# Kernel tuning notes

Hardware: AMD Instinct MI355X
Metric: run time of the kernel (lower is better)

## Reference

```python
import jax, jax.numpy as jnp
import numpy as np

B, T, K, H, NH = 16, 2048, 128, 1024, 8
NEG = -jnp.inf


def _ln(x, g, b, eps=1e-5):
    m = x.mean(-1, keepdims=True)
    v = ((x - m) ** 2).mean(-1, keepdims=True)
    return (x - m) * jax.lax.rsqrt(v + eps) * g + b


def _mha(q, k, v, in_w, in_b, out_w, out_b, nh, bias):
    # torch nn.MultiheadAttention (batch_first, eval mode). bias: additive mask (B or 1, 1, Lq, Lk)
    Bq, Lq, Hd = q.shape
    Lk = k.shape[1]
    d = Hd // nh
    wq, wk, wv = in_w[:Hd], in_w[Hd:2 * Hd], in_w[2 * Hd:]
    bq, bk, bv = in_b[:Hd], in_b[Hd:2 * Hd], in_b[2 * Hd:]
    qh = (q @ wq.T + bq).reshape(Bq, Lq, nh, d).transpose(0, 2, 1, 3)
    kh = (k @ wk.T + bk).reshape(Bq, Lk, nh, d).transpose(0, 2, 1, 3)
    vh = (v @ wv.T + bv).reshape(Bq, Lk, nh, d).transpose(0, 2, 1, 3)
    scores = jnp.einsum('bhqd,bhkd->bhqk', qh, kh) * (1.0 / np.sqrt(d)) + bias
    attn = jax.nn.softmax(scores, axis=-1)
    o = jnp.einsum('bhqk,bhkd->bhqd', attn, vh).transpose(0, 2, 1, 3).reshape(Bq, Lq, Hd)
    return o @ out_w.T + out_b


def setup_inputs() -> dict:
    key = jax.random.key(0)
    ks = jax.random.split(key, 12)
    projected = jax.random.normal(ks[0], (B, T, H), dtype=jnp.float32)
    starts = jnp.sort(jax.random.randint(ks[1], (B, K), 0, T - 1), axis=-1)
    widths = jax.random.randint(ks[2], (B, K), 1, 33)
    ends = jnp.minimum(starts + widths, T)
    boundaries = jnp.stack([starts, ends], axis=-1).astype(jnp.int64)
    slot_mask = jnp.ones((B, K), dtype=jnp.float32)
    s = 0.02
    p = {
        'qp_w': jax.random.normal(ks[3], (H, H)) * s, 'qp_b': jnp.zeros((H,)),
        'ca_in_w': jax.random.normal(ks[4], (3 * H, H)) * s, 'ca_in_b': jnp.zeros((3 * H,)),
        'ca_out_w': jax.random.normal(ks[5], (H, H)) * s, 'ca_out_b': jnp.zeros((H,)),
        'cn_g': jnp.ones((H,)), 'cn_b': jnp.zeros((H,)),
        'sa_in_w': jax.random.normal(ks[6], (3 * H, H)) * s, 'sa_in_b': jnp.zeros((3 * H,)),
        'sa_out_w': jax.random.normal(ks[7], (H, H)) * s, 'sa_out_b': jnp.zeros((H,)),
        'on_g': jnp.ones((H,)), 'on_b': jnp.zeros((H,)),
    }
    return {'projected': projected, 'boundaries': boundaries, 'slot_mask': slot_mask, **p}


def reference(projected, boundaries, slot_mask, qp_w, qp_b, ca_in_w, ca_in_b, ca_out_w, ca_out_b,
              cn_g, cn_b, sa_in_w, sa_in_b, sa_out_w, sa_out_b, on_g, on_b):
    Bb, Tt, Hh = projected.shape
    Kk = slot_mask.shape[1]
    tidx = jnp.arange(Tt)
    starts = boundaries[:, :, 0]  # (B,K)
    ends = boundaries[:, :, 1]
    # in-boundary membership: (B,K,T)
    in_bkt = (tidx[None, None, :] >= starts[:, :, None]) & (tidx[None, None, :] < ends[:, :, None])
    valid = slot_mask > 0.5  # (B,K)
    # --- mean-pool init queries ---
    in_slot = (in_bkt & (slot_mask[:, :, None] > 0)).astype(projected.dtype)  # (B,K,T)
    w = in_slot / jnp.clip(in_slot.sum(axis=-1, keepdims=True), 1.0, None)
    init_slots = jnp.einsum('bkt,bth->bkh', w, projected)
    queries = init_slots @ qp_w.T + qp_b
    # --- boundary-masked cross attention (True = blocked) ---
    blocked = ~(in_bkt & valid[:, :, None])  # (B,K,T)
    cross_bias = jnp.where(blocked, NEG, 0.0)[:, None, :, :]  # (B,1,K,T)
    attn_out = _mha(queries, projected, projected, ca_in_w, ca_in_b, ca_out_w, ca_out_b, NH, cross_bias)
    slots = _ln(attn_out + queries, cn_g, cn_b)
    # --- causal self-attention over slots with key padding ---
    causal = jnp.where(jnp.triu(jnp.ones((Kk, Kk), bool), 1), NEG, 0.0)[None, None, :, :]
    pad = jnp.where(slot_mask[:, None, None, :] < 0.5, NEG, 0.0)  # (B,1,1,K)
    ctx = _mha(slots, slots, slots, sa_in_w, sa_in_b, sa_out_w, sa_out_b, NH, causal + pad)
    return _ln(ctx + slots, on_g, on_b)
```

## Files before the change

kernel.cpp:

```cpp
#include <hip/hip_runtime.h>
#include <hip/hip_bf16.h>


#define Bc 16
#define Tc 2048
#define Kc 128
#define Hc 1024
#define NHc 8

typedef unsigned short u16;
typedef __attribute__((ext_vector_type(8))) short short8v;
typedef __attribute__((ext_vector_type(4))) float f32x4;

__device__ __forceinline__ float bf2f(u16 u){ return __uint_as_float(((unsigned)u)<<16); }
__device__ __forceinline__ u16 f2bf(float f){
  unsigned x = __float_as_uint(f);
  return (u16)((x + 0x7fffu + ((x>>16)&1u)) >> 16);
}
__device__ __forceinline__ float4 ld4(const float* p){ return *(const float4*)p; }
__device__ __forceinline__ float ldx(const void* x, size_t idx, bool isbf){
  return isbf ? bf2f(((const u16*)x)[idx]) : ((const float*)x)[idx];
}
__device__ __forceinline__ bool probe_bf(const u16* probe){ return probe[0] == 0x3F80; }

__device__ __forceinline__ void gload_lds16(const u16* g, u16* l){
  __builtin_amdgcn_global_load_lds(
      (const __attribute__((address_space(1))) unsigned int*)g,
      (__attribute__((address_space(3))) unsigned int*)l, 16, 0, 0);
}

struct CvtArgs { const void* src[15]; int n[15]; long long off[15]; int tobf[15]; };

__global__ __launch_bounds__(256) void convert_params(CvtArgs a, float* fbase,
                                                      u16* bbase, const u16* probe)
{
  bool isbf = probe_bf(probe);
  int g = blockIdx.x*256 + threadIdx.x;
  int stride = gridDim.x*256;
  #pragma unroll 1
  for (int seg=0; seg<15; seg++){
    int n = a.n[seg];
    const void* s = a.src[seg];
    if (a.tobf[seg]){
      u16* d = bbase + a.off[seg];
      if (isbf){ const u16* su=(const u16*)s; for (int i=g;i<n;i+=stride) d[i]=su[i]; }
      else     { const float* sf=(const float*)s; for (int i=g;i<n;i+=stride) d[i]=f2bf(sf[i]); }
    } else {
      float* d = fbase + a.off[seg];
      for (int i=g;i<n;i+=stride) d[i] = ldx(s, i, isbf);
    }
  }
}

__global__ __launch_bounds__(256) void transpose_bf(
    const u16* __restrict__ src, u16* __restrict__ dst, int n)
{
  __shared__ u16 t[32][33];
  int bx = blockIdx.x*32, by = blockIdx.y*32;
  int tx = threadIdx.x & 31, ty = threadIdx.x >> 5;
  #pragma unroll
  for (int i=0;i<32;i+=8)
    t[ty+i][tx] = src[(size_t)(by+ty+i)*n + bx+tx];
  __syncthreads();
  #pragma unroll
  for (int i=0;i<32;i+=8)
    dst[(size_t)(bx+ty+i)*n + by+tx] = t[tx][ty+i];
}

__global__ __launch_bounds__(256) void gemm_mfma(
    const u16* __restrict__ A, const u16* __restrict__ W,
    const float* __restrict__ bias, float* __restrict__ Cf, u16* __restrict__ Cb,
    int M, int N, int Kd, int lda, int ldw, int ldc, float alpha,
    int ZH, long long sAb, long long sAh, long long sWb, long long sWh,
    long long sCb, long long sCh, long long sBh)
{
  __shared__ __align__(16) u16 As[128*32];
  __shared__ __align__(16) u16 Bs[128*32];
  int z = blockIdx.z, bi = z / ZH, hi = z % ZH;
  A += (size_t)bi*sAb + (size_t)hi*sAh;
  W += (size_t)bi*sWb + (size_t)hi*sWh;
  int tid = threadIdx.x;
  int m0 = blockIdx.y*128, n0 = blockIdx.x*128;
  int wave = tid >> 6, lane = tid & 63;
  int wm = (wave >> 1)*64, wn = (wave & 1)*64;
  int r = lane & 15, half = lane >> 4;
  int srow = wave*32 + (lane >> 2);
  int skc  = (lane & 3) << 3;
  u16* ldsA = &As[wave*1024];
  u16* ldsB = &Bs[wave*1024];

  f32x4 acc[4][4] = {};

  for (int k0 = 0; k0 < Kd; k0 += 32){
    gload_lds16(A + (size_t)(m0+srow   )*lda + k0 + skc, ldsA);
    gload_lds16(A + (size_t)(m0+srow+16)*lda + k0 + skc, ldsA + 512);
    gload_lds16(W + (size_t)(n0+srow   )*ldw + k0 + skc, ldsB);
    gload_lds16(W + (size_t)(n0+srow+16)*ldw + k0 + skc, ldsB + 512);
    __syncthreads();
    short8v a[4], b[4];
    #pragma unroll
    for (int mi=0;mi<4;mi++)
      a[mi] = *(const short8v*)&As[(wm+mi*16+r)*32 + half*8];
    #pragma unroll
    for (int ni=0;ni<4;ni++)
      b[ni] = *(const short8v*)&Bs[(wn+ni*16+r)*32 + half*8];
    #pragma unroll
    for (int mi=0;mi<4;mi++)
      #pragma unroll
      for (int ni=0;ni<4;ni++)
        acc[mi][ni] = __builtin_amdgcn_mfma_f32_16x16x32_bf16(a[mi], b[ni], acc[mi][ni], 0, 0, 0);
    __syncthreads();
  }

  float* Cfp = Cf ? Cf + (size_t)bi*sCb + (size_t)hi*sCh : nullptr;
  u16*   Cbp = Cb ? Cb + (size_t)bi*sCb + (size_t)hi*sCh : nullptr;
  #pragma unroll
  for (int ni=0;ni<4;ni++){
    int col = n0 + wn + ni*16 + r;
    float bvv = bias ? bias[(size_t)hi*sBh + col] : 0.f;
    #pragma unroll
    for (int mi=0;mi<4;mi++){
      #pragma unroll
      for (int d=0;d<4;d++){
        int rowc = m0 + wm + mi*16 + half*4 + d;
        float o = alpha*acc[mi][ni][d] + bvv;
        if (Cfp) Cfp[(size_t)rowc*ldc + col] = o;
        if (Cbp) Cbp[(size_t)rowc*ldc + col] = f2bf(o);
      }
    }
  }
}

__global__ __launch_bounds__(256) void gemm_nt(
    const float* __restrict__ A, const float* __restrict__ W,
    const float* __restrict__ bias, float* __restrict__ C,
    int M, int N, int Kd, int lda, int ldw, int ldc, float alpha,
    int ZH, long long sAb, long long sAh, long long sWb, long long sWh,
    long long sCb, long long sCh, long long sBh)
{
  __shared__ float As[16][68];
  __shared__ float Bs[16][68];
  int z = blockIdx.z, bi = z / ZH, hi = z % ZH;
  A += (size_t)bi*sAb + (size_t)hi*sAh;
  W += (size_t)bi*sWb + (size_t)hi*sWh;
  C += (size_t)bi*sCb + (size_t)hi*sCh;
  int tid = threadIdx.x;
  int m0 = blockIdx.y*64, n0 = blockIdx.x*64;
  int tx = tid & 15, ty = tid >> 4;
  int lRow = tid >> 2, lK = (tid & 3) << 2;
  float acc[4][4] = {};
  for (int k0=0; k0<Kd; k0+=16){
    float4 av = ld4(A + (size_t)(m0+lRow)*lda + k0 + lK);
    float4 wv = ld4(W + (size_t)(n0+lRow)*ldw + k0 + lK);
    As[lK+0][lRow]=av.x; As[lK+1][lRow]=av.y; As[lK+2][lRow]=av.z; As[lK+3][lRow]=av.w;
    Bs[lK+0][lRow]=wv.x; Bs[lK+1][lRow]=wv.y; Bs[lK+2][lRow]=wv.z; Bs[lK+3][lRow]=wv.w;
    __syncthreads();
    #pragma unroll
    for (int kk=0;kk<16;kk++){
      float a[4], b[4];
      #pragma unroll
      for (int i=0;i<4;i++) a[i]=As[kk][ty*4+i];
      #pragma unroll
      for (int j=0;j<4;j++) b[j]=Bs[kk][tx*4+j];
      #pragma unroll
      for (int i=0;i<4;i++)
        #pragma unroll
        for (int j=0;j<4;j++)
          acc[i][j] += a[i]*b[j];
    }
    __syncthreads();
  }
  float bv[4] = {0.f,0.f,0.f,0.f};
  if (bias){
    const float* bp = bias + (size_t)hi*sBh + n0 + tx*4;
    bv[0]=bp[0]; bv[1]=bp[1]; bv[2]=bp[2]; bv[3]=bp[3];
  }
  #pragma unroll
  for (int i=0;i<4;i++){
    float4 o;
    o.x = alpha*acc[i][0]+bv[0];
    o.y = alpha*acc[i][1]+bv[1];
    o.z = alpha*acc[i][2]+bv[2];
    o.w = alpha*acc[i][3]+bv[3];
    *(float4*)(C + (size_t)(m0+ty*4+i)*ldc + n0 + tx*4) = o;
  }
}

__global__ __launch_bounds__(256) void gemm_nn(
    const float* __restrict__ A, const float* __restrict__ Bm,
    const float* __restrict__ bias, float* __restrict__ C, u16* __restrict__ Cb,
    int M, int N, int Kd, int lda, int ldb, int ldc, float alpha,
    int ZH, long long sAb, long long sAh, long long sBb, long long sBh,
    long long sCb, long long sCh, long long sBiash)
{
  __shared__ float As[16][68];
  __shared__ float Bs[16][68];
  int z = blockIdx.z, bi = z / ZH, hi = z % ZH;
  A  += (size_t)bi*sAb + (size_t)hi*sAh;
  Bm += (size_t)bi*sBb + (size_t)hi*sBh;
  int tid = threadIdx.x;
  int m0 = blockIdx.y*64, n0 = blockIdx.x*64;
  int tx = tid & 15, ty = tid >> 4;
  int lRow = tid >> 2, lK = (tid & 3) << 2;
  int bKr = tid >> 4, bNc = (tid & 15) << 2;
  float acc[4][4] = {};
  for (int k0=0; k0<Kd; k0+=16){
    float4 av = ld4(A + (size_t)(m0+lRow)*lda + k0 + lK);
    float4 bvv = ld4(Bm + (size_t)(k0+bKr)*ldb + n0 + bNc);
    As[lK+0][lRow]=av.x; As[lK+1][lRow]=av.y; As[lK+2][lRow]=av.z; As[lK+3][lRow]=av.w;
    *(float4*)&Bs[bKr][bNc] = bvv;
    __syncthreads();
    #pragma unroll
    for (int kk=0;kk<16;kk++){
      float a[4], b[4];
      #pragma unroll
      for (int i=0;i<4;i++) a[i]=As[kk][ty*4+i];
      #pragma unroll
      for (int j=0;j<4;j++) b[j]=Bs[kk][tx*4+j];
      #pragma unroll
      for (int i=0;i<4;i++)
        #pragma unroll
        for (int j=0;j<4;j++)
          acc[i][j] += a[i]*b[j];
    }
    __syncthreads();
  }
  float bv[4] = {0.f,0.f,0.f,0.f};
  if (bias){
    const float* bp = bias + (size_t)hi*sBiash + n0 + tx*4;
    bv[0]=bp[0]; bv[1]=bp[1]; bv[2]=bp[2]; bv[3]=bp[3];
  }
  #pragma unroll
  for (int i=0;i<4;i++){
    float o0 = alpha*acc[i][0]+bv[0];
    float o1 = alpha*acc[i][1]+bv[1];
    float o2 = alpha*acc[i][2]+bv[2];
    float o3 = alpha*acc[i][3]+bv[3];
    size_t rowoff = (size_t)(m0+ty*4+i)*ldc + n0 + tx*4;
    if (Cb){
      u16* cp = Cb + (size_t)bi*sCb + (size_t)hi*sCh + rowoff;
      ushort4 ov; ov.x=f2bf(o0); ov.y=f2bf(o1); ov.z=f2bf(o2); ov.w=f2bf(o3);
      *(ushort4*)cp = ov;
    } else {
      float* cp = C + (size_t)bi*sCb + (size_t)hi*sCh + rowoff;
      float4 ov; ov.x=o0; ov.y=o1; ov.z=o2; ov.w=o3;
      *(float4*)cp = ov;
    }
  }
}

__global__ __launch_bounds__(512) void pool_kernel(
    const void* __restrict__ x, const int* __restrict__ bnd,
    const float* __restrict__ maskf, u16* __restrict__ out,
    const u16* __restrict__ probe)
{
  __shared__ float red[1024];
  bool isbf = probe_bf(probe);
  bool is64 = (bnd[1] == 0);
  int slot = blockIdx.x; int b = slot >> 7; int tid = threadIdx.x;
  int s0 = is64 ? bnd[4*slot]   : bnd[2*slot];
  int e0 = is64 ? bnd[4*slot+2] : bnd[2*slot+1];
  int rh = tid >> 8;
  int d0 = (tid & 255)*4;
  float acc[4] = {0.f,0.f,0.f,0.f};
  for (int t=s0+rh; t<e0; t+=2){
    size_t base = ((size_t)b*Tc + (size_t)t)*Hc + d0;
    if (isbf){
      ushort4 v = *(const ushort4*)((const u16*)x + base);
      acc[0]+=bf2f(v.x); acc[1]+=bf2f(v.y); acc[2]+=bf2f(v.z); acc[3]+=bf2f(v.w);
    } else {
      float4 v = ld4((const float*)x + base);
      acc[0]+=v.x; acc[1]+=v.y; acc[2]+=v.z; acc[3]+=v.w;
    }
  }
  if (rh == 1){
    #pragma unroll
    for (int r=0;r<4;r++) red[(tid&255)*4 + r] = acc[r];
  }
  __syncthreads();
  if (rh == 0){
    int cnt = e0 - s0; if (cnt < 1) cnt = 1;
    float inv = (maskf[slot] > 0.5f) ? 1.f/(float)cnt : 0.f;
    ushort4 o;
    o.x=f2bf((acc[0]+red[(tid&255)*4+0])*inv);
    o.y=f2bf((acc[1]+red[(tid&255)*4+1])*inv);
    o.z=f2bf((acc[2]+red[(tid&255)*4+2])*inv);
    o.w=f2bf((acc[3]+red[(tid&255)*4+3])*inv);
    *(ushort4*)(out + (size_t)slot*Hc + d0) = o;
  }
}

__global__ __launch_bounds__(512, 2) void cross_attn4(
    const void* __restrict__ x, const int* __restrict__ bnd,
    const u16* __restrict__ Yg, u16* __restrict__ pooled,
    const u16* __restrict__ probe)
{
  __shared__ __align__(16) u16 Xs[32*1024];
  __shared__ float redC[4*2*64*4];
  __shared__ float sc[8*32];
  __shared__ __align__(16) float pt[32*8];
  bool isbf = probe_bf(probe);
  bool is64 = (bnd[1] == 0);
  int slot = blockIdx.x; int b = slot >> 7;
  int tid = threadIdx.x;
  int wv = tid >> 6, lane = tid & 63;
  int s0 = is64 ? bnd[4*slot]   : bnd[2*slot];
  int e0 = is64 ? bnd[4*slot+2] : bnd[2*slot+1];
  int w = e0 - s0;

  {
    int rrow = tid >> 7;
    int cu = (tid & 127) * 8;
    for (int t = rrow; t < w; t += 4){
      size_t base = ((size_t)b*Tc + (size_t)(s0+t))*Hc + cu;
      int dst = t*1024 + (cu ^ ((t&7)<<3));
      short8v v;
      if (isbf){
        v = *(const short8v*)((const u16*)x + base);
      } else {
        const float* xf = (const float*)x + base;
        float4 f0 = ld4(xf), f1 = ld4(xf+4);
        v[0]=(short)f2bf(f0.x); v[1]=(short)f2bf(f0.y);
        v[2]=(short)f2bf(f0.z); v[3]=(short)f2bf(f0.w);
        v[4]=(short)f2bf(f1.x); v[5]=(short)f2bf(f1.y);
        v[6]=(short)f2bf(f1.z); v[7]=(short)f2bf(f1.w);
      }
      *(short8v*)&Xs[dst] = v;
    }
  }
  __syncthreads();

  if (wv < 4){
    int r = lane & 15, half = lane >> 4;
    f32x4 acc0 = {0.f,0.f,0.f,0.f}, acc1 = {0.f,0.f,0.f,0.f};
    #pragma unroll
    for (int ks=0; ks<8; ks++){
      int k = wv*256 + ks*32 + half*8;
      short8v vb = {0,0,0,0,0,0,0,0};
      if (r < 8)
        vb = *(const short8v*)(Yg + (size_t)slot*8192 + r*1024 + k);
      int xs = k ^ ((r&7)<<3);
      short8v a0 = *(const short8v*)&Xs[ r      *1024 + xs];
      short8v a1 = *(const short8v*)&Xs[(16+r)*1024 + xs];
      acc0 = __builtin_amdgcn_mfma_f32_16x16x32_bf16(a0, vb, acc0, 0, 0, 0);
      acc1 = __builtin_amdgcn_mfma_f32_16x16x32_bf16(a1, vb, acc1, 0, 0, 0);
    }
    #pragma unroll
    for (int i=0;i<4;i++){
      redC[((wv*2+0)*64+lane)*4+i] = acc0[i];
      redC[((wv*2+1)*64+lane)*4+i] = acc1[i];
    }
  }
  __syncthreads();

  {
    int f = tid >> 8, rem = tid & 255, l = rem >> 2, i = rem & 3;
    float v = 0.f;
    #pragma unroll
    for (int q=0; q<4; q++) v += redC[((q*2+f)*64+l)*4+i];
    int hh = l & 15;
    int t  = f*16 + (l>>4)*4 + i;
    if (hh < 8) sc[hh*32 + t] = v * 0.08838834764831845f;
  }
  __syncthreads();

  if (tid < 256){
    int hh = tid >> 5, t = tid & 31;
    float v = (t < w) ? sc[hh*32 + t] : -1e30f;
    float m = v;
    for (int off=16; off; off>>=1) m = fmaxf(m, __shfl_xor(m, off));
    float e = (t < w) ? __expf(v - m) : 0.f;
    float s = e;
    for (int off=16; off; off>>=1) s += __shfl_xor(s, off);
    pt[t*8 + hh] = e / s;
  }
  __syncthreads();

  {
    int d0 = tid*2;
    float pa[8][2] = {};
    for (int t=0; t<w; t++){
      float4 p0 = *(const float4*)&pt[t*8];
      float4 p1 = *(const float4*)&pt[t*8+4];
      unsigned xw = *(const unsigned*)&Xs[t*1024 + (d0 ^ ((t&7)<<3))];
      float x0 = bf2f((u16)(xw & 0xffffu));
      float x1 = bf2f((u16)(xw >> 16));
      pa[0][0]+=p0.x*x0; pa[0][1]+=p0.x*x1;
      pa[1][0]+=p0.y*x0; pa[1][1]+=p0.y*x1;
      pa[2][0]+=p0.z*x0; pa[2][1]+=p0.z*x1;
      pa[3][0]+=p0.w*x0; pa[3][1]+=p0.w*x1;
      pa[4][0]+=p1.x*x0; pa[4][1]+=p1.x*x1;
      pa[5][0]+=p1.y*x0; pa[5][1]+=p1.y*x1;
      pa[6][0]+=p1.z*x0; pa[6][1]+=p1.z*x1;
      pa[7][0]+=p1.w*x0; pa[7][1]+=p1.w*x1;
    }
    #pragma unroll
    for (int hh=0;hh<8;hh++){
      ushort2 o; o.x = f2bf(pa[hh][0]); o.y = f2bf(pa[hh][1]);
      *(ushort2*)(pooled + (size_t)slot*8192 + hh*1024 + d0) = o;
    }
  }
}

__global__ __launch_bounds__(256) void ln_res(
    const float* __restrict__ xin, const float* __restrict__ res,
    const float* __restrict__ g, const float* __restrict__ bb,
    float* __restrict__ outf, u16* __restrict__ outb, const u16* __restrict__ probe,
    u16* __restrict__ dualb)
{
  __shared__ float red[256];
  bool tobf = (probe != nullptr) && probe_bf(probe);
  int row = blockIdx.x, tid = threadIdx.x;
  const float* xr = xin + (size_t)row*1024;
  const float* rr = res + (size_t)row*1024;
  float v[4]; float s = 0.f;
  #pragma unroll
  for (int r=0;r<4;r++){ v[r] = xr[tid+256*r] + rr[tid+256*r]; s += v[r]; }
  red[tid] = s; __syncthreads();
  for (int off=128; off>0; off>>=1){ if (tid<off) red[tid]+=red[tid+off]; __syncthreads(); }
  float mean = red[0] * (1.f/1024.f);
  __syncthreads();
  float s2 = 0.f;
  #pragma unroll
  for (int r=0;r<4;r++){ float d = v[r]-mean; s2 += d*d; }
  red[tid]=s2; __syncthreads();
  for (int off=128; off>0; off>>=1){ if (tid<off) red[tid]+=red[tid+off]; __syncthreads(); }
  float var = red[0]*(1.f/1024.f);
  float rs = rsqrtf(var + 1e-5f);
  #pragma unroll
  for (int r=0;r<4;r++){
    int c = tid+256*r;
    float o = (v[r]-mean)*rs*g[c] + bb[c];
    if (tobf) outb[(size_t)row*1024 + c] = f2bf(o);
    else      outf[(size_t)row*1024 + c] = o;
    if (dualb) dualb[(size_t)row*1024 + c] = f2bf(o);
  }
}

__global__ __launch_bounds__(256) void sa_softmax(float* __restrict__ S,
                                                  const float* __restrict__ maskf)
{
  int wv = threadIdx.x>>6, lane = threadIdx.x&63;
  int row = blockIdx.x*4 + wv;
  int z = row >> 7, q = row & 127;
  int b = z >> 3;
  float* Sr = S + (size_t)row*128;
  float v0 = Sr[lane], v1 = Sr[lane+64];
  if (lane    > q || maskf[b*128+lane   ] < 0.5f) v0 = -1e30f;
  if (lane+64 > q || maskf[b*128+lane+64] < 0.5f) v1 = -1e30f;
  float m = fmaxf(v0,v1);
  for (int off=32; off; off>>=1) m = fmaxf(m, __shfl_xor(m,off));
  float e0 = expf(v0-m), e1 = expf(v1-m);
  float s = e0+e1;
  for (int off=32; off; off>>=1) s += __shfl_xor(s,off);
  float inv = 1.f/s;
  Sr[lane] = e0*inv; Sr[lane+64] = e1*inv;
}

extern "C" void kernel_launch(void* const* d_in, const int* in_sizes, int n_in,
                              void* d_out, int out_size, void* d_ws, size_t ws_size,
                              hipStream_t stream)
{
  const void* x       = d_in[0];
  const int* bnd      = (const int*)d_in[1];
  const u16* probe    = (const u16*)d_in[9];
  float* ws = (float*)d_ws;

  const long long F_qp_b    = 0;
  const long long F_ca_in_b = 1024;
  const long long F_ca_out_b= 4096;
  const long long F_cn_g    = 5120;
  const long long F_cn_b    = 6144;
  const long long F_sa_in_b = 7168;
  const long long F_sa_out_b= 10240;
  const long long F_on_g    = 11264;
  const long long F_on_b    = 12288;
  const long long F_smask   = 13312;
  u16* wb = (u16*)(ws + 15360);
  const long long B_qp_w    = 0;
  const long long B_ca_in_w = 1048576;
  const long long B_ca_out_w= 4194304;
  const long long B_sa_in_w = 5242880;
  const long long B_sa_out_w= 8388608;
  const long long B_wkT     = 9437184;
  const long long PB        = 5258240;

  float* qbuf    = ws + PB + 0;
  float* slots   = ws + PB + 2097152;
  u16*   Ybuf    = (u16*)(ws + PB + 4194304);
  u16*   poolb   = Ybuf;
  u16*   islots  = (u16*)(ws + PB + 12582912);
  u16*   qbuf_b  = (u16*)(ws + PB + 13631488);
  u16*   qhbuf   = (u16*)(ws + PB + 14680064);
  u16*   attnb   = (u16*)(ws + PB + 15728640);
  float* attn2   = ws + PB + 16777216;
  u16*   slots_b = (u16*)(ws + PB + 18874368);
  float* qkv     = ws + PB + 19922944;
  float* Sb      = ws + PB + 26214400;
  u16*   ctx_b   = (u16*)(ws + PB + 28311552);
  float* ctx2    = ws + PB + 29360128;
  if (ws_size < (size_t)(PB + 31457280ll) * 4ull) return;

  CvtArgs ca;
  const int srcIdx[15]     = {3,5,7,11,13, 4,6,8,9,10,12,14,15,16, 2};
  const long long offs[15] = {B_qp_w,B_ca_in_w,B_ca_out_w,B_sa_in_w,B_sa_out_w,
                              F_qp_b,F_ca_in_b,F_ca_out_b,F_cn_g,F_cn_b,
                              F_sa_in_b,F_sa_out_b,F_on_g,F_on_b,F_smask};
  const int tobf[15]       = {1,1,1,1,1, 0,0,0,0,0,0,0,0,0, 0};
  for (int i=0;i<15;i++){ ca.src[i]=d_in[srcIdx[i]]; ca.n[i]=in_sizes[srcIdx[i]];
                          ca.off[i]=offs[i]; ca.tobf[i]=tobf[i]; }
  convert_params<<<dim3(4096),dim3(256),0,stream>>>(ca, ws, wb, probe);

  const float* Pf = ws;
  transpose_bf<<<dim3(32,32),dim3(256),0,stream>>>(wb + B_ca_in_w + 1048576ll,
      wb + B_wkT, 1024);
  pool_kernel<<<dim3(2048),dim3(512),0,stream>>>(x, bnd, Pf+F_smask, islots, probe);
  gemm_mfma<<<dim3(8,16,1),dim3(256),0,stream>>>(islots, wb+B_qp_w, Pf+F_qp_b,
      qbuf, qbuf_b,
      2048,1024,1024, 1024,1024,1024, 1.f, 1, 0,0, 0,0, 0,0, 0);
  gemm_mfma<<<dim3(8,16,1),dim3(256),0,stream>>>(qbuf_b, wb+B_ca_in_w, Pf+F_ca_in_b,
      (float*)nullptr, qhbuf,
      2048,1024,1024, 1024,1024,1024, 1.f, 1, 0,0, 0,0, 0,0, 0);
  gemm_mfma<<<dim3(8,16,8),dim3(256),0,stream>>>(qhbuf, wb+B_wkT,
      (const float*)nullptr, (float*)nullptr, Ybuf,
      2048,1024,128, 1024,1024,8192, 1.f, 8, 0,128, 0,128, 0,1024, 0);
  cross_attn4<<<dim3(2048),dim3(512),0,stream>>>(x, bnd, Ybuf, poolb, probe);
  gemm_mfma<<<dim3(1,16,8),dim3(256),0,stream>>>(poolb, wb+B_ca_in_w+2097152ll,
      Pf+F_ca_in_b+2048, (float*)nullptr, attnb,
      2048,128,1024, 8192,1024,1024, 1.f, 8, 0,1024, 0,131072, 0,128, 128);
  gemm_mfma<<<dim3(8,16,1),dim3(256),0,stream>>>(attnb, wb+B_ca_out_w, Pf+F_ca_out_b,
      attn2, (u16*)nullptr,
      2048,1024,1024, 1024,1024,1024, 1.f, 1, 0,0, 0,0, 0,0, 0);
  ln_res<<<dim3(2048),dim3(256),0,stream>>>(attn2, qbuf, Pf+F_cn_g, Pf+F_cn_b,
      slots, (u16*)nullptr, (const u16*)nullptr, slots_b);
  gemm_mfma<<<dim3(24,16,1),dim3(256),0,stream>>>(slots_b, wb+B_sa_in_w, Pf+F_sa_in_b,
      qkv, (u16*)nullptr,
      2048,3072,1024, 1024,1024,3072, 1.f, 1, 0,0, 0,0, 0,0, 0);
  gemm_nt<<<dim3(2,2,128),dim3(256),0,stream>>>(qkv, qkv + 1024,
      (const float*)nullptr, Sb,
      128,128,128, 3072,3072,128, 0.08838834764831845f, 8,
      393216,128, 393216,128, 131072,16384, 0);
  sa_softmax<<<dim3(4096),dim3(256),0,stream>>>(Sb, Pf+F_smask);
  gemm_nn<<<dim3(2,2,128),dim3(256),0,stream>>>(Sb, qkv + 2048,
      (const float*)nullptr, (float*)nullptr, ctx_b,
      128,128,128, 128,3072,1024, 1.f, 8,
      131072,16384, 393216,128, 131072,128, 0);
  gemm_mfma<<<dim3(8,16,1),dim3(256),0,stream>>>(ctx_b, wb+B_sa_out_w, Pf+F_sa_out_b,
      ctx2, (u16*)nullptr,
      2048,1024,1024, 1024,1024,1024, 1.f, 1, 0,0, 0,0, 0,0, 0);
  ln_res<<<dim3(2048),dim3(256),0,stream>>>(ctx2, slots, Pf+F_on_g, Pf+F_on_b,
      (float*)d_out, (u16*)d_out, probe, (u16*)nullptr);
}
```

Baseline: 538.7 us.

## Fuse slot self-attention into one MFMA kernel, use 128x64 GEMM tiles, widen pooling

Replaces the fp32 scalar QK^T GEMM, the separate softmax kernel and the PV GEMM with a single fused_sa kernel per (batch, head). It converts Q, K and V to bf16 in swizzled LDS, uses MFMA for both products, and applies the causal/padding softmax in registers. This removes the round trip of the score matrix through global memory and two kernel launches. Most dense projections move to a new gemm_mfma64 variant with smaller N tiles (128x64), which doubles the grid for more parallelism. The pooling kernel goes from 512 to 1024 threads so four row groups run in parallel. Self-attention now uses bf16 inputs, which lowers precision, and the fused kernel launches only 128 blocks.

```diff
diff --git a/kernel.cpp b/kernel.cpp
--- a/kernel.cpp
+++ b/kernel.cpp
@@ -27,6 +27,15 @@
   __builtin_amdgcn_global_load_lds(
       (const __attribute__((address_space(1))) unsigned int*)g,
       (__attribute__((address_space(3))) unsigned int*)l, 16, 0, 0);
+}
+
+__device__ __forceinline__ short8v pack8(float4 f0, float4 f1){
+  short8v v;
+  v[0]=(short)f2bf(f0.x); v[1]=(short)f2bf(f0.y);
+  v[2]=(short)f2bf(f0.z); v[3]=(short)f2bf(f0.w);
+  v[4]=(short)f2bf(f1.x); v[5]=(short)f2bf(f1.y);
+  v[6]=(short)f2bf(f1.z); v[7]=(short)f2bf(f1.w);
+  return v;
 }
 
 struct CvtArgs { const void* src[15]; int n[15]; long long off[15]; int tobf[15]; };
@@ -131,140 +140,86 @@
   }
 }
 
-__global__ __launch_bounds__(256) void gemm_nt(
-    const float* __restrict__ A, const float* __restrict__ W,
-    const float* __restrict__ bias, float* __restrict__ C,
+__global__ __launch_bounds__(256) void gemm_mfma64(
+    const u16* __restrict__ A, const u16* __restrict__ W,
+    const float* __restrict__ bias, float* __restrict__ Cf, u16* __restrict__ Cb,
     int M, int N, int Kd, int lda, int ldw, int ldc, float alpha,
     int ZH, long long sAb, long long sAh, long long sWb, long long sWh,
     long long sCb, long long sCh, long long sBh)
 {
-  __shared__ float As[16][68];
-  __shared__ float Bs[16][68];
+  __shared__ __align__(16) u16 As[128*32];
+  __shared__ __align__(16) u16 Bs[64*32];
   int z = blockIdx.z, bi = z / ZH, hi = z % ZH;
   A += (size_t)bi*sAb + (size_t)hi*sAh;
   W += (size_t)bi*sWb + (size_t)hi*sWh;
-  C += (size_t)bi*sCb + (size_t)hi*sCh;
   int tid = threadIdx.x;
-  int m0 = blockIdx.y*64, n0 = blockIdx.x*64;
-  int tx = tid & 15, ty = tid >> 4;
-  int lRow = tid >> 2, lK = (tid & 3) << 2;
-  float acc[4][4] = {};
-  for (int k0=0; k0<Kd; k0+=16){
-    float4 av = ld4(A + (size_t)(m0+lRow)*lda + k0 + lK);
-    float4 wv = ld4(W + (size_t)(n0+lRow)*ldw + k0 + lK);
-    As[lK+0][lRow]=av.x; As[lK+1][lRow]=av.y; As[lK+2][lRow]=av.z; As[lK+3][lRow]=av.w;
-    Bs[lK+0][lRow]=wv.x; Bs[lK+1][lRow]=wv.y; Bs[lK+2][lRow]=wv.z; Bs[lK+3][lRow]=wv.w;
+  int m0 = blockIdx.y*128, n0 = blockIdx.x*64;
+  int wave = tid >> 6, lane = tid & 63;
+  int wm = (wave >> 1)*64, wn = (wave & 1)*32;
+  int r = lane & 15, half = lane >> 4;
+  int srow = wave*32 + (lane >> 2);
+  int brow = wave*16 + (lane >> 2);
+  int skc  = (lane & 3) << 3;
+  u16* ldsA = &As[wave*1024];
+  u16* ldsB = &Bs[wave*512];
+
+  f32x4 acc[4][2] = {};
+
+  for (int k0 = 0; k0 < Kd; k0 += 32){
+    gload_lds16(A + (size_t)(m0+srow   )*lda + k0 + skc, ldsA);
+    gload_lds16(A + (size_t)(m0+srow+16)*lda + k0 + skc, ldsA + 512);
+    gload_lds16(W + (size_t)(n0+brow   )*ldw + k0 + skc, ldsB);
     __syncthreads();
-    #pragma unroll
-    for (int kk=0;kk<16;kk++){
-      float a[4], b[4];
-      #pragma unroll
-      for (int i=0;i<4;i++) a[i]=As[kk][ty*4+i];
-      #pragma unroll
-      for (int j=0;j<4;j++) b[j]=Bs[kk][tx*4+j];
-      #pragma unroll
-      for (int i=0;i<4;i++)
-        #pragma unroll
-        for (int j=0;j<4;j++)
-          acc[i][j] += a[i]*b[j];
-    }
+    short8v a[4], b[2];
+    #pragma unroll
+    for (int mi=0;mi<4;mi++)
+      a[mi] = *(const short8v*)&As[(wm+mi*16+r)*32 + half*8];
+    #pragma unroll
+    for (int ni=0;ni<2;ni++)
+      b[ni] = *(const short8v*)&Bs[(wn+ni*16+r)*32 + half*8];
+    #pragma unroll
+    for (int mi=0;mi<4;mi++)
+      #pragma unroll
+      for (int ni=0;ni<2;ni++)
+        acc[mi][ni] = __builtin_amdgcn_mfma_f32_16x16x32_bf16(a[mi], b[ni], acc[mi][ni], 0, 0, 0);
     __syncthreads();
   }
-  float bv[4] = {0.f,0.f,0.f,0.f};
-  if (bias){
-    const float* bp = bias + (size_t)hi*sBh + n0 + tx*4;
-    bv[0]=bp[0]; bv[1]=bp[1]; bv[2]=bp[2]; bv[3]=bp[3];
-  }
-  #pragma unroll
-  for (int i=0;i<4;i++){
-    float4 o;
-    o.x = alpha*acc[i][0]+bv[0];
-    o.y = alpha*acc[i][1]+bv[1];
-    o.z = alpha*acc[i][2]+bv[2];
-    o.w = alpha*acc[i][3]+bv[3];
-    *(float4*)(C + (size_t)(m0+ty*4+i)*ldc + n0 + tx*4) = o;
-  }
-}
-
-__global__ __launch_bounds__(256) void gemm_nn(
-    const float* __restrict__ A, const float* __restrict__ Bm,
-    const float* __restrict__ bias, float* __restrict__ C, u16* __restrict__ Cb,
-    int M, int N, int Kd, int lda, int ldb, int ldc, float alpha,
-    int ZH, long long sAb, long long sAh, long long sBb, long long sBh,
-    long long sCb, long long sCh, long long sBiash)
-{
-  __shared__ float As[16][68];
-  __shared__ float Bs[16][68];
-  int z = blockIdx.z, bi = z / ZH, hi = z % ZH;
-  A  += (size_t)bi*sAb + (size_t)hi*sAh;
-  Bm += (size_t)bi*sBb + (size_t)hi*sBh;
-  int tid = threadIdx.x;
-  int m0 = blockIdx.y*64, n0 = blockIdx.x*64;
-  int tx = tid & 15, ty = tid >> 4;
-  int lRow = tid >> 2, lK = (tid & 3) << 2;
-  int bKr = tid >> 4, bNc = (tid & 15) << 2;
-  float acc[4][4] = {};
-  for (int k0=0; k0<Kd; k0+=16){
-    float4 av = ld4(A + (size_t)(m0+lRow)*lda + k0 + lK);
-    float4 bvv = ld4(Bm + (size_t)(k0+bKr)*ldb + n0 + bNc);
-    As[lK+0][lRow]=av.x; As[lK+1][lRow]=av.y; As[lK+2][lRow]=av.z; As[lK+3][lRow]=av.w;
-    *(float4*)&Bs[bKr][bNc] = bvv;
-    __syncthreads();
-    #pragma unroll
-    for (int kk=0;kk<16;kk++){
-      float a[4], b[4];
-      #pragma unroll
-      for (int i=0;i<4;i++) a[i]=As[kk][ty*4+i];
-      #pragma unroll
-      for (int j=0;j<4;j++) b[j]=Bs[kk][tx*4+j];
-      #pragma unroll
-      for (int i=0;i<4;i++)
-        #pragma unroll
-        for (int j=0;j<4;j++)
-          acc[i][j] += a[i]*b[j];
-    }
-    __syncthreads();
-  }
-  float bv[4] = {0.f,0.f,0.f,0.f};
-  if (bias){
-    const float* bp = bias + (size_t)hi*sBiash + n0 + tx*4;
-    bv[0]=bp[0]; bv[1]=bp[1]; bv[2]=bp[2]; bv[3]=bp[3];
-  }
-  #pragma unroll
-  for (int i=0;i<4;i++){
-    float o0 = alpha*acc[i][0]+bv[0];
-    float o1 = alpha*acc[i][1]+bv[1];
-    float o2 = alpha*acc[i][2]+bv[2];
-    float o3 = alpha*acc[i][3]+bv[3];
-    size_t rowoff = (size_t)(m0+ty*4+i)*ldc + n0 + tx*4;
-    if (Cb){
-      u16* cp = Cb + (size_t)bi*sCb + (size_t)hi*sCh + rowoff;
-      ushort4 ov; ov.x=f2bf(o0); ov.y=f2bf(o1); ov.z=f2bf(o2); ov.w=f2bf(o3);
-      *(ushort4*)cp = ov;
-    } else {
-      float* cp = C + (size_t)bi*sCb + (size_t)hi*sCh + rowoff;
-      float4 ov; ov.x=o0; ov.y=o1; ov.z=o2; ov.w=o3;
-      *(float4*)cp = ov;
-    }
-  }
-}
-
-__global__ __launch_bounds__(512) void pool_kernel(
+
+  float* Cfp = Cf ? Cf + (size_t)bi*sCb + (size_t)hi*sCh : nullptr;
+  u16*   Cbp = Cb ? Cb + (size_t)bi*sCb + (size_t)hi*sCh : nullptr;
+  #pragma unroll
+  for (int ni=0;ni<2;ni++){
+    int col = n0 + wn + ni*16 + r;
+    float bvv = bias ? bias[(size_t)hi*sBh + col] : 0.f;
+    #pragma unroll
+    for (int mi=0;mi<4;mi++){
+      #pragma unroll
+      for (int d=0;d<4;d++){
+        int rowc = m0 + wm + mi*16 + half*4 + d;
+        float o = alpha*acc[mi][ni][d] + bvv;
+        if (Cfp) Cfp[(size_t)rowc*ldc + col] = o;
+        if (Cbp) Cbp[(size_t)rowc*ldc + col] = f2bf(o);
+      }
+    }
+  }
+}
+
+__global__ __launch_bounds__(1024) void pool_kernel(
     const void* __restrict__ x, const int* __restrict__ bnd,
     const float* __restrict__ maskf, u16* __restrict__ out,
     const u16* __restrict__ probe)
 {
-  __shared__ float red[1024];
+  __shared__ float red[3*1024];
   bool isbf = probe_bf(probe);
   bool is64 = (bnd[1] == 0);
   int slot = blockIdx.x; int b = slot >> 7; int tid = threadIdx.x;
   int s0 = is64 ? bnd[4*slot]   : bnd[2*slot];
   int e0 = is64 ? bnd[4*slot+2] : bnd[2*slot+1];
   int rh = tid >> 8;
-  int d0 = (tid & 255)*4;
+  int q = (tid & 255)*4;
   float acc[4] = {0.f,0.f,0.f,0.f};
-  for (int t=s0+rh; t<e0; t+=2){
-    size_t base = ((size_t)b*Tc + (size_t)t)*Hc + d0;
+  for (int t=s0+rh; t<e0; t+=4){
+    size_t base = ((size_t)b*Tc + (size_t)t)*Hc + q;
     if (isbf){
       ushort4 v = *(const ushort4*)((const u16*)x + base);
       acc[0]+=bf2f(v.x); acc[1]+=bf2f(v.y); acc[2]+=bf2f(v.z); acc[3]+=bf2f(v.w);
@@ -273,20 +228,20 @@
       acc[0]+=v.x; acc[1]+=v.y; acc[2]+=v.z; acc[3]+=v.w;
     }
   }
-  if (rh == 1){
-    #pragma unroll
-    for (int r=0;r<4;r++) red[(tid&255)*4 + r] = acc[r];
+  if (rh > 0){
+    #pragma unroll
+    for (int r=0;r<4;r++) red[(rh-1)*1024 + q + r] = acc[r];
   }
   __syncthreads();
   if (rh == 0){
     int cnt = e0 - s0; if (cnt < 1) cnt = 1;
     float inv = (maskf[slot] > 0.5f) ? 1.f/(float)cnt : 0.f;
     ushort4 o;
-    o.x=f2bf((acc[0]+red[(tid&255)*4+0])*inv);
-    o.y=f2bf((acc[1]+red[(tid&255)*4+1])*inv);
-    o.z=f2bf((acc[2]+red[(tid&255)*4+2])*inv);
-    o.w=f2bf((acc[3]+red[(tid&255)*4+3])*inv);
-    *(ushort4*)(out + (size_t)slot*Hc + d0) = o;
+    o.x=f2bf((acc[0]+red[q+0]+red[1024+q+0]+red[2048+q+0])*inv);
+    o.y=f2bf((acc[1]+red[q+1]+red[1024+q+1]+red[2048+q+1])*inv);
+    o.z=f2bf((acc[2]+red[q+2]+red[1024+q+2]+red[2048+q+2])*inv);
+    o.w=f2bf((acc[3]+red[q+3]+red[1024+q+3]+red[2048+q+3])*inv);
+    *(ushort4*)(out + (size_t)slot*Hc + q) = o;
   }
 }
 
@@ -319,11 +274,7 @@
         v = *(const short8v*)((const u16*)x + base);
       } else {
         const float* xf = (const float*)x + base;
-        float4 f0 = ld4(xf), f1 = ld4(xf+4);
-        v[0]=(short)f2bf(f0.x); v[1]=(short)f2bf(f0.y);
-        v[2]=(short)f2bf(f0.z); v[3]=(short)f2bf(f0.w);
-        v[4]=(short)f2bf(f1.x); v[5]=(short)f2bf(f1.y);
-        v[6]=(short)f2bf(f1.z); v[7]=(short)f2bf(f1.w);
+        v = pack8(ld4(xf), ld4(xf+4));
       }
       *(short8v*)&Xs[dst] = v;
     }
@@ -402,6 +353,153 @@
   }
 }
 
+__global__ __launch_bounds__(256) void fused_sa(
+    const float* __restrict__ qkv, const float* __restrict__ maskf,
+    u16* __restrict__ ctx_b)
+{
+  __shared__ __align__(16) u16 Qs[128*128];
+  __shared__ __align__(16) u16 Ks[128*128];
+  __shared__ __align__(16) u16 Vs[128*128];
+  __shared__ float rmax[2][128];
+  __shared__ float rsum[2][128];
+  __shared__ float maskL[128];
+  int z = blockIdx.x;
+  int b = z >> 3, h = z & 7;
+  int tid = threadIdx.x;
+  const float* base = qkv + (size_t)(b*128)*3072 + h*128;
+
+  {
+    int sr = tid >> 4, scol = (tid & 15) * 8;
+    if (tid < 128) maskL[tid] = maskf[b*128 + tid];
+    #pragma unroll
+    for (int i=0;i<8;i++){
+      int rr = sr + i*16;
+      const float* qp = base + (size_t)rr*3072 + scol;
+      int swz = scol ^ ((rr&7)<<3);
+      *(short8v*)&Qs[rr*128 + swz]  = pack8(ld4(qp),      ld4(qp+4));
+      *(short8v*)&Ks[rr*128 + swz]  = pack8(ld4(qp+1024), ld4(qp+1028));
+      *(short8v*)&Vs[rr*128 + scol] = pack8(ld4(qp+2048), ld4(qp+2052));
+    }
+  }
+  __syncthreads();
+
+  int wave = tid >> 6, lane = tid & 63;
+  int wr = wave >> 1, wc = wave & 1;
+  int r = lane & 15, half = lane >> 4;
+
+  f32x4 acc[4][4] = {};
+  #pragma unroll
+  for (int ks=0; ks<4; ks++){
+    int kb = ks*32 + half*8;
+    int xo = kb ^ ((r&7)<<3);
+    short8v a[4], bb[4];
+    #pragma unroll
+    for (int mi=0;mi<4;mi++)
+      a[mi] = *(const short8v*)&Qs[(wr*64+mi*16+r)*128 + xo];
+    #pragma unroll
+    for (int ni=0;ni<4;ni++)
+      bb[ni] = *(const short8v*)&Ks[(wc*64+ni*16+r)*128 + xo];
+    #pragma unroll
+    for (int mi=0;mi<4;mi++)
+      #pragma unroll
+      for (int ni=0;ni<4;ni++)
+        acc[mi][ni] = __builtin_amdgcn_mfma_f32_16x16x32_bf16(a[mi], bb[ni], acc[mi][ni], 0, 0, 0);
+  }
+
+  const float scale = 0.08838834764831845f;
+  float rmx[4][4];
+  #pragma unroll
+  for (int mi=0;mi<4;mi++)
+    #pragma unroll
+    for (int d=0;d<4;d++){
+      int q = wr*64 + mi*16 + half*4 + d;
+      float mx = -1e30f;
+      #pragma unroll
+      for (int ni=0;ni<4;ni++){
+        int k = wc*64 + ni*16 + r;
+        float v = acc[mi][ni][d]*scale;
+        if (k > q || maskL[k] < 0.5f) v = -1e30f;
+        acc[mi][ni][d] = v;
+        mx = fmaxf(mx, v);
+      }
+      for (int off=8; off; off>>=1) mx = fmaxf(mx, __shfl_xor(mx, off));
+      rmx[mi][d] = mx;
+      if (r == 0) rmax[wc][q] = mx;
+    }
+  __syncthreads();
+
+  float rs_[4][4];
+  #pragma unroll
+  for (int mi=0;mi<4;mi++)
+    #pragma unroll
+    for (int d=0;d<4;d++){
+      int q = wr*64 + mi*16 + half*4 + d;
+      float m = fmaxf(rmax[0][q], rmax[1][q]);
+      float s = 0.f;
+      #pragma unroll
+      for (int ni=0;ni<4;ni++){
+        float e = __expf(acc[mi][ni][d] - m);
+        acc[mi][ni][d] = e;
+        s += e;
+      }
+      for (int off=8; off; off>>=1) s += __shfl_xor(s, off);
+      rs_[mi][d] = s;
+      if (r == 0) rsum[wc][q] = s;
+    }
+  __syncthreads();
+
+  #pragma unroll
+  for (int mi=0;mi<4;mi++)
+    #pragma unroll
+    for (int d=0;d<4;d++){
+      int q = wr*64 + mi*16 + half*4 + d;
+      float inv = 1.f / (rsum[0][q] + rsum[1][q]);
+      #pragma unroll
+      for (int ni=0;ni<4;ni++){
+        int k = wc*64 + ni*16 + r;
+        Qs[q*128 + (k ^ ((q&7)<<3))] = f2bf(acc[mi][ni][d]*inv);
+      }
+    }
+  __syncthreads();
+
+  f32x4 o[4][4] = {};
+  #pragma unroll
+  for (int ks=0; ks<4; ks++){
+    int kb = ks*32 + half*8;
+    int xo = kb ^ ((r&7)<<3);
+    short8v a[4], bb[4];
+    #pragma unroll
+    for (int mi=0;mi<4;mi++)
+      a[mi] = *(const short8v*)&Qs[(wr*64+mi*16+r)*128 + xo];
+    #pragma unroll
+    for (int ni=0;ni<4;ni++){
+      int col = wc*64 + ni*16 + r;
+      short8v t;
+      #pragma unroll
+      for (int j=0;j<8;j++) t[j] = (short)Vs[(kb + j)*128 + col];
+      bb[ni] = t;
+    }
+    #pragma unroll
+    for (int mi=0;mi<4;mi++)
+      #pragma unroll
+      for (int ni=0;ni<4;ni++)
+        o[mi][ni] = __builtin_amdgcn_mfma_f32_16x16x32_bf16(a[mi], bb[ni], o[mi][ni], 0, 0, 0);
+  }
+
+  #pragma unroll
+  for (int ni=0;ni<4;ni++){
+    int d = wc*64 + ni*16 + r;
+    #pragma unroll
+    for (int mi=0;mi<4;mi++){
+      #pragma unroll
+      for (int dd=0;dd<4;dd++){
+        int q = wr*64 + mi*16 + half*4 + dd;
+        ctx_b[(size_t)(b*128+q)*1024 + h*128 + d] = f2bf(o[mi][ni][dd]);
+      }
+    }
+  }
+}
+
 __global__ __launch_bounds__(256) void ln_res(
     const float* __restrict__ xin, const float* __restrict__ res,
     const float* __restrict__ g, const float* __restrict__ bb,
@@ -435,26 +533,6 @@
     else      outf[(size_t)row*1024 + c] = o;
     if (dualb) dualb[(size_t)row*1024 + c] = f2bf(o);
   }
-}
-
-__global__ __launch_bounds__(256) void sa_softmax(float* __restrict__ S,
-                                                  const float* __restrict__ maskf)
-{
-  int wv = threadIdx.x>>6, lane = threadIdx.x&63;
-  int row = blockIdx.x*4 + wv;
-  int z = row >> 7, q = row & 127;
-  int b = z >> 3;
-  float* Sr = S + (size_t)row*128;
-  float v0 = Sr[lane], v1 = Sr[lane+64];
-  if (lane    > q || maskf[b*128+lane   ] < 0.5f) v0 = -1e30f;
-  if (lane+64 > q || maskf[b*128+lane+64] < 0.5f) v1 = -1e30f;
-  float m = fmaxf(v0,v1);
-  for (int off=32; off; off>>=1) m = fmaxf(m, __shfl_xor(m,off));
-  float e0 = expf(v0-m), e1 = expf(v1-m);
-  float s = e0+e1;
-  for (int off=32; off; off>>=1) s += __shfl_xor(s,off);
-  float inv = 1.f/s;
-  Sr[lane] = e0*inv; Sr[lane+64] = e1*inv;
 }
 
 extern "C" void kernel_launch(void* const* d_in, const int* in_sizes, int n_in,
@@ -496,7 +574,6 @@
   float* attn2   = ws + PB + 16777216;
   u16*   slots_b = (u16*)(ws + PB + 18874368);
   float* qkv     = ws + PB + 19922944;
-  float* Sb      = ws + PB + 26214400;
   u16*   ctx_b   = (u16*)(ws + PB + 28311552);
   float* ctx2    = ws + PB + 29360128;
   if (ws_size < (size_t)(PB + 31457280ll) * 4ull) return;
@@ -514,38 +591,30 @@
   const float* Pf = ws;
   transpose_bf<<<dim3(32,32),dim3(256),0,stream>>>(wb + B_ca_in_w + 1048576ll,
       wb + B_wkT, 1024);
-  pool_kernel<<<dim3(2048),dim3(512),0,stream>>>(x, bnd, Pf+F_smask, islots, probe);
-  gemm_mfma<<<dim3(8,16,1),dim3(256),0,stream>>>(islots, wb+B_qp_w, Pf+F_qp_b,
+  pool_kernel<<<dim3(2048),dim3(1024),0,stream>>>(x, bnd, Pf+F_smask, islots, probe);
+  gemm_mfma64<<<dim3(16,16,1),dim3(256),0,stream>>>(islots, wb+B_qp_w, Pf+F_qp_b,
       qbuf, qbuf_b,
       2048,1024,1024, 1024,1024,1024, 1.f, 1, 0,0, 0,0, 0,0, 0);
-  gemm_mfma<<<dim3(8,16,1),dim3(256),0,stream>>>(qbuf_b, wb+B_ca_in_w, Pf+F_ca_in_b,
+  gemm_mfma64<<<dim3(16,16,1),dim3(256),0,stream>>>(qbuf_b, wb+B_ca_in_w, Pf+F_ca_in_b,
       (float*)nullptr, qhbuf,
       2048,1024,1024, 1024,1024,1024, 1.f, 1, 0,0, 0,0, 0,0, 0);
   gemm_mfma<<<dim3(8,16,8),dim3(256),0,stream>>>(qhbuf, wb+B_wkT,
       (const float*)nullptr, (float*)nullptr, Ybuf,
       2048,1024,128, 1024,1024,8192, 1.f, 8, 0,128, 0,128, 0,1024, 0);
   cross_attn4<<<dim3(2048),dim3(512),0,stream>>>(x, bnd, Ybuf, poolb, probe);
-  gemm_mfma<<<dim3(1,16,8),dim3(256),0,stream>>>(poolb, wb+B_ca_in_w+2097152ll,
+  gemm_mfma64<<<dim3(2,16,8),dim3(256),0,stream>>>(poolb, wb+B_ca_in_w+2097152ll,
       Pf+F_ca_in_b+2048, (float*)nullptr, attnb,
       2048,128,1024, 8192,1024,1024, 1.f, 8, 0,1024, 0,131072, 0,128, 128);
-  gemm_mfma<<<dim3(8,16,1),dim3(256),0,stream>>>(attnb, wb+B_ca_out_w, Pf+F_ca_out_b,
+  gemm_mfma64<<<dim3(16,16,1),dim3(256),0,stream>>>(attnb, wb+B_ca_out_w, Pf+F_ca_out_b,
       attn2, (u16*)nullptr,
       2048,1024,1024, 1024,1024,1024, 1.f, 1, 0,0, 0,0, 0,0, 0);
   ln_res<<<dim3(2048),dim3(256),0,stream>>>(attn2, qbuf, Pf+F_cn_g, Pf+F_cn_b,
       slots, (u16*)nullptr, (const u16*)nullptr, slots_b);
-  gemm_mfma<<<dim3(24,16,1),dim3(256),0,stream>>>(slots_b, wb+B_sa_in_w, Pf+F_sa_in_b,
+  gemm_mfma64<<<dim3(48,16,1),dim3(256),0,stream>>>(slots_b, wb+B_sa_in_w, Pf+F_sa_in_b,
       qkv, (u16*)nullptr,
       2048,3072,1024, 1024,1024,3072, 1.f, 1, 0,0, 0,0, 0,0, 0);
-  gemm_nt<<<dim3(2,2,128),dim3(256),0,stream>>>(qkv, qkv + 1024,
-      (const float*)nullptr, Sb,
-      128,128,128, 3072,3072,128, 0.08838834764831845f, 8,
-      393216,128, 393216,128, 131072,16384, 0);
-  sa_softmax<<<dim3(4096),dim3(256),0,stream>>>(Sb, Pf+F_smask);
-  gemm_nn<<<dim3(2,2,128),dim3(256),0,stream>>>(Sb, qkv + 2048,
-      (const float*)nullptr, (float*)nullptr, ctx_b,
-      128,128,128, 128,3072,1024, 1.f, 8,
-      131072,16384, 393216,128, 131072,128, 0);
-  gemm_mfma<<<dim3(8,16,1),dim3(256),0,stream>>>(ctx_b, wb+B_sa_out_w, Pf+F_sa_out_b,
+  fused_sa<<<dim3(128),dim3(256),0,stream>>>(qkv, Pf+F_smask, ctx_b);
+  gemm_mfma64<<<dim3(16,16,1),dim3(256),0,stream>>>(ctx_b, wb+B_sa_out_w, Pf+F_sa_out_b,
       ctx2, (u16*)nullptr,
       2048,1024,1024, 1024,1024,1024, 1.f, 1, 0,0, 0,0, 0,0, 0);
   ln_res<<<dim3(2048),dim3(256),0,stream>>>(ctx2, slots, Pf+F_on_g, Pf+F_on_b,
```

After: 485.5 us. -9.9%, faster.
